# Kernel optimization log

Hardware: AMD Instinct MI355X
Metric: run time of the kernel (lower is better)

Reference implementation:

```python
import jax, jax.numpy as jnp
import numpy as np

EMB_DIM = 1024
NUM_HEADS = 16
HEAD_DIM = EMB_DIM // NUM_HEADS
B, S_Q, S_KV = 4, 2048, 2048


def setup_inputs() -> dict:
    key = jax.random.key(0)
    ks = jax.random.split(key, 12)
    s = EMB_DIM ** -0.5  # torch Linear default init scale (approx, uniform-like)
    inp = {
        "q": jax.random.normal(ks[0], (B, S_Q, EMB_DIM), jnp.float32),
        "k": jax.random.normal(ks[1], (B, S_KV, EMB_DIM), jnp.float32),
        "v": jax.random.normal(ks[2], (B, S_KV, EMB_DIM), jnp.float32),
        "mask": jax.random.randint(ks[3], (B, S_KV), 0, 2, jnp.int32),
        "Wq": jax.random.normal(ks[4], (EMB_DIM, EMB_DIM), jnp.float32) * s,
        "bq": jnp.zeros((EMB_DIM,), jnp.float32),
        "Wk": jax.random.normal(ks[5], (EMB_DIM, EMB_DIM), jnp.float32) * s,
        "bk": jnp.zeros((EMB_DIM,), jnp.float32),
        "Wv": jax.random.normal(ks[6], (EMB_DIM, EMB_DIM), jnp.float32) * s,
        "bv": jnp.zeros((EMB_DIM,), jnp.float32),
        "Wo": jax.random.normal(ks[7], (EMB_DIM, EMB_DIM), jnp.float32) * s,
        "bo": jnp.zeros((EMB_DIM,), jnp.float32),
    }
    return inp


def reference(q, k, v, mask, Wq, bq, Wk, bk, Wv, bv, Wo, bo):
    Bsz, Sq, E = q.shape
    Skv = k.shape[1]
    H, D = NUM_HEADS, HEAD_DIM
    scale = D ** -0.5

    # projections (torch Linear: x @ W.T + b)
    qh = (q @ Wq.T + bq).reshape(Bsz, Sq, H, D).transpose(0, 2, 1, 3)   # [B,H,Sq,D]
    kh = (k @ Wk.T + bk).reshape(Bsz, Skv, H, D).transpose(0, 2, 1, 3)  # [B,H,Skv,D]
    vh = (v @ Wv.T + bv).reshape(Bsz, Skv, H, D).transpose(0, 2, 1, 3)  # [B,H,Skv,D]

    attn = jnp.einsum("bhqd,bhkd->bhqk", qh, kh) * scale  # [B,H,Sq,Skv]

    valid = mask != 0                                      # [B,Skv]
    all_invalid = ~jnp.any(valid, axis=-1, keepdims=True)  # [B,1]
    safe = valid | all_invalid                             # reopened rows
    attn = jnp.where(safe[:, None, None, :], attn, -jnp.inf)

    attn = jax.nn.softmax(attn, axis=-1)
    attn = jnp.where(all_invalid.reshape(Bsz, 1, 1, 1), 0.0, attn)

    out = jnp.einsum("bhqk,bhkd->bhqd", attn, vh)          # [B,H,Sq,D]
    out = out.transpose(0, 2, 1, 3).reshape(Bsz, Sq, E)
    return out @ Wo.T + bo
```

## Files before the change

kernel.cpp:

```cpp
#include <hip/hip_runtime.h>
#include <hip/hip_bf16.h>

typedef short bh8 __attribute__((ext_vector_type(8)));
typedef float f32x4 __attribute__((ext_vector_type(4)));
typedef float f32x16 __attribute__((ext_vector_type(16)));
typedef float f2 __attribute__((ext_vector_type(2)));
typedef unsigned int uint4v __attribute__((ext_vector_type(4)));

#define GLOBAL_P(p) ((const __attribute__((address_space(1))) void*)(p))
#define LDS_P(p)    ((__attribute__((address_space(3))) void*)(p))

__device__ inline bh8 pack8(const float4& a, const float4& b) {
    union { bh8 v; __hip_bfloat16 h[8]; } u;
    u.h[0] = __float2bfloat16(a.x); u.h[1] = __float2bfloat16(a.y);
    u.h[2] = __float2bfloat16(a.z); u.h[3] = __float2bfloat16(a.w);
    u.h[4] = __float2bfloat16(b.x); u.h[5] = __float2bfloat16(b.y);
    u.h[6] = __float2bfloat16(b.z); u.h[7] = __float2bfloat16(b.w);
    return u.v;
}

__global__ __launch_bounds__(256) void cvt1(
    const float* __restrict__ a, __hip_bfloat16* __restrict__ oa)
{
    size_t i = ((size_t)blockIdx.x * 256 + threadIdx.x) * 8;
    float4 x0 = *(const float4*)(a + i), x1 = *(const float4*)(a + i + 4);
    *(bh8*)(oa + i) = pack8(x0, x1);
}

__global__ __launch_bounds__(256) void cvtW(
    const float* __restrict__ a, const float* __restrict__ b,
    const float* __restrict__ c, const float* __restrict__ d,
    __hip_bfloat16* __restrict__ o)
{
    int seg = blockIdx.x >> 9;
    const float* src = (seg == 0) ? a : (seg == 1) ? b : (seg == 2) ? c : d;
    size_t i = ((size_t)(blockIdx.x & 511) * 256 + threadIdx.x) * 8;
    float4 x0 = *(const float4*)(src + i), x1 = *(const float4*)(src + i + 4);
    *(bh8*)(o + (size_t)seg * 1048576 + i) = pack8(x0, x1);
}

__global__ __launch_bounds__(256) void maskScan(
    const int* __restrict__ mask, int* __restrict__ idx, int* __restrict__ nv)
{
    __shared__ int ts[256];
    const int b = blockIdx.x, tid = threadIdx.x;
    int f[8], cnt = 0;
#pragma unroll
    for (int j = 0; j < 8; ++j) {
        f[j] = (mask[b * 2048 + tid * 8 + j] != 0) ? 1 : 0;
        cnt += f[j];
    }
    ts[tid] = cnt;
    __syncthreads();
    for (int off = 1; off < 256; off <<= 1) {
        int v = (tid >= off) ? ts[tid - off] : 0;
        __syncthreads();
        ts[tid] += v;
        __syncthreads();
    }
    int base = ts[tid] - cnt;
#pragma unroll
    for (int j = 0; j < 8; ++j)
        if (f[j]) idx[b * 2048 + base++] = tid * 8 + j;
    if (tid == 255) nv[b] = ts[255];
}

__global__ __launch_bounds__(256) void gatherTok(
    const float* __restrict__ kf, const float* __restrict__ vf,
    const int* __restrict__ idx, const int* __restrict__ nv,
    __hip_bfloat16* __restrict__ kc, __hip_bfloat16* __restrict__ vc)
{
    const int b = blockIdx.x >> 5, rb = blockIdx.x & 31;
    const int n = nv[b], np = (n + 127) & ~127;
    const int r = rb * 64 + (threadIdx.x >> 2);
    if (r >= np) return;
    const int c0 = (threadIdx.x & 3) * 256;
    bh8* dk = (bh8*)(kc + ((size_t)b * 2048 + r) * 1024 + c0);
    bh8* dv = (bh8*)(vc + ((size_t)b * 2048 + r) * 1024 + c0);
    if (r < n) {
        const int s = idx[b * 2048 + r];
        const float4* sk = (const float4*)(kf + ((size_t)b * 2048 + s) * 1024 + c0);
        const float4* sv = (const float4*)(vf + ((size_t)b * 2048 + s) * 1024 + c0);
#pragma unroll
        for (int i = 0; i < 32; ++i) {
            dk[i] = pack8(sk[2 * i], sk[2 * i + 1]);
            dv[i] = pack8(sv[2 * i], sv[2 * i + 1]);
        }
    } else {
        bh8 z = {};
#pragma unroll
        for (int i = 0; i < 32; ++i) { dk[i] = z; dv[i] = z; }
    }
}

template <typename TC, bool COMPACT>
__global__ __launch_bounds__(256) void gemm_bt(
    const __hip_bfloat16* __restrict__ A, const __hip_bfloat16* __restrict__ W,
    const float* __restrict__ bias, TC* __restrict__ C,
    int M, int N, int Ksz, float oscale, const int* __restrict__ nvp)
{
    __shared__ __hip_bfloat16 As[128 * 64];
    __shared__ __hip_bfloat16 Bs[128 * 64];
    const int tid = threadIdx.x;
    const int l = tid & 63, w = tid >> 6;
    const int g4 = l >> 4, rl = l & 15;
    const int nb = N >> 7;
    const int bm = blockIdx.x / nb, bn = blockIdx.x % nb;
    if constexpr (COMPACT) {
        const int np = (nvp[bm >> 4] + 127) & ~127;
        if ((bm & 15) * 128 >= np) return;
    }
    const long m0 = (long)bm * 128, n0 = (long)bn * 128;

    const __hip_bfloat16* ag[4];
    const __hip_bfloat16* wg[4];
    int ldsbase[4];
#pragma unroll
    for (int i = 0; i < 4; ++i) {
        int c = i * 256 + tid;
        int row = c >> 3, c8 = c & 7;
        ag[i] = A + (m0 + row) * Ksz + c8 * 8;
        wg[i] = W + (n0 + row) * Ksz + c8 * 8;
        ldsbase[i] = (i * 256 + w * 64) * 8;
    }

    const int wr = w >> 1, wc = w & 1;
    f32x4 acc[4][4];
#pragma unroll
    for (int i = 0; i < 4; ++i)
#pragma unroll
        for (int j = 0; j < 4; ++j) acc[i][j] = f32x4{0.f, 0.f, 0.f, 0.f};

    const int nk = Ksz >> 6;
    for (int t = 0; t < nk; ++t) {
        __syncthreads();
#pragma unroll
        for (int i = 0; i < 4; ++i) {
            __builtin_amdgcn_global_load_lds(GLOBAL_P(ag[i]), LDS_P((__hip_bfloat16*)As + ldsbase[i]), 16, 0, 0);
            __builtin_amdgcn_global_load_lds(GLOBAL_P(wg[i]), LDS_P((__hip_bfloat16*)Bs + ldsbase[i]), 16, 0, 0);
            ag[i] += 64; wg[i] += 64;
        }
        __syncthreads();
#pragma unroll
        for (int kc = 0; kc < 2; ++kc) {
            bh8 af[4], bf[4];
#pragma unroll
            for (int mt = 0; mt < 4; ++mt) {
                int row = wr * 64 + mt * 16 + rl;
                af[mt] = *(const bh8*)(As + row * 64 + 8 * g4 + 32 * kc);
            }
#pragma unroll
            for (int nt = 0; nt < 4; ++nt) {
                int row = wc * 64 + nt * 16 + rl;
                bf[nt] = *(const bh8*)(Bs + row * 64 + 8 * g4 + 32 * kc);
            }
#pragma unroll
            for (int mt = 0; mt < 4; ++mt)
#pragma unroll
                for (int nt = 0; nt < 4; ++nt)
                    acc[mt][nt] = __builtin_amdgcn_mfma_f32_16x16x32_bf16(af[mt], bf[nt], acc[mt][nt], 0, 0, 0);
        }
    }

    float bv[4];
#pragma unroll
    for (int nt = 0; nt < 4; ++nt)
        bv[nt] = bias[n0 + wc * 64 + nt * 16 + rl];
#pragma unroll
    for (int mt = 0; mt < 4; ++mt) {
#pragma unroll
        for (int r = 0; r < 4; ++r) {
            long row = m0 + wr * 64 + mt * 16 + g4 * 4 + r;
            TC* cp = C + row * N + n0 + wc * 64 + rl;
#pragma unroll
            for (int nt = 0; nt < 4; ++nt) {
                float x = (acc[mt][nt][r] + bv[nt]) * oscale;
                if constexpr (__is_same(TC, float)) cp[nt * 16] = x;
                else cp[nt * 16] = __float2bfloat16(x);
            }
        }
    }
}

#define THRL 11.0f

__global__ __launch_bounds__(256, 2) void attn_kernel(
    const __hip_bfloat16* __restrict__ Qm, const __hip_bfloat16* __restrict__ Km,
    const __hip_bfloat16* __restrict__ Vm, const int* __restrict__ nvp,
    __hip_bfloat16* __restrict__ Om)
{
    __shared__ __hip_bfloat16 Kt[2][64 * 64];
    __shared__ __hip_bfloat16 Vt[2][64 * 64];
    __shared__ float biasS[2048];
    const int tid = threadIdx.x;
    const int w = tid >> 6, l = tid & 63;
    const int G = l >> 5, c = l & 31;
    const int id = blockIdx.x;
    const int xcd = id & 7, slot = id >> 3;
    const int bh = xcd * 8 + (slot >> 4);
    const int qb = slot & 15;
    const int b = bh >> 4, h = bh & 15;
    const int q0 = qb * 128 + w * 32;

    const int n = nvp[b];
    const int nt = (n + 63) >> 6;

#pragma unroll
    for (int i = 0; i < 8; ++i) {
        int idx = i * 256 + tid;
        biasS[idx] = (idx < n) ? 0.f : -1e30f;
    }

    const __hip_bfloat16* qp = Qm + (size_t)(b * 2048 + q0 + c) * 1024 + h * 64 + 8 * G;
    bh8 qf[4];
#pragma unroll
    for (int kc = 0; kc < 4; ++kc) qf[kc] = *(const bh8*)(qp + 16 * kc);

    const int l38 = l >> 3, lc8 = l & 7;
    const __hip_bfloat16* kg0 = Km + (size_t)(b * 2048 + 16 * w + l38) * 1024 + h * 64 + 8 * ((lc8 ^ l38 ^ (2 * w)) & 7);
    const __hip_bfloat16* kg1 = Km + (size_t)(b * 2048 + 16 * w + 8 + l38) * 1024 + h * 64 + 8 * ((lc8 ^ l38 ^ (2 * w + 1)) & 7);
    const int kbase_e = w * 1024;

    const int vpi = tid >> 3, vd0 = (tid & 7) * 8;
    const __hip_bfloat16* vbase = Vm + (size_t)(b * 2048 + 2 * vpi) * 1024 + h * 64 + vd0;

    bh8 va0, va1;
    auto loadV = [&](int tt) {
        const __hip_bfloat16* vp = vbase + (size_t)tt * 64 * 1024;
        va0 = *(const bh8*)vp;
        va1 = *(const bh8*)(vp + 1024);
    };
    auto stageV = [&](int buf) {
        __hip_bfloat16* dst = &Vt[buf][0];
#pragma unroll
        for (int j = 0; j < 8; ++j) {
            int d = vd0 + j;
            int swz = ((d & 7) ^ (d >> 3)) << 3;
            unsigned lo = (unsigned short)((const short*)&va0)[j];
            unsigned hi = (unsigned short)((const short*)&va1)[j];
            *(unsigned*)&dst[(d * 64 + 2 * vpi) ^ swz] = lo | (hi << 16);
        }
    };
    auto stageK = [&](int buf, int tt) {
        const size_t off = (size_t)tt * 64 * 1024;
        __builtin_amdgcn_global_load_lds(GLOBAL_P(kg0 + off), LDS_P(&Kt[buf][0] + kbase_e), 16, 0, 0);
        __builtin_amdgcn_global_load_lds(GLOBAL_P(kg1 + off), LDS_P(&Kt[buf][0] + kbase_e + 512), 16, 0, 0);
    };

    stageK(0, 0);
    loadV(0);
    stageV(0);
    loadV(nt > 1 ? 1 : 0);
    __syncthreads();

    f32x16 o0 = {0.f}, o1 = {0.f};
    float m_run = -1e29f, l_run = 0.f;

    for (int t = 0; t < nt; ++t) {
        const int buf = t & 1;
        if (t < nt - 1) {
            stageK(buf ^ 1, t + 1);
            stageV(buf ^ 1);
            loadV(t + 2 < nt ? t + 2 : nt - 1);
        }
        __builtin_amdgcn_sched_barrier(0);

        const __hip_bfloat16* kbuf = &Kt[buf][0];
        const int kx0 = ((c & 7) ^ (c >> 3)) << 3;
        const int kx1 = kx0 ^ 32;
        f32x16 s0 = {0.f}, s1 = {0.f};
        __builtin_amdgcn_s_setprio(1);
#pragma unroll
        for (int kc = 0; kc < 4; ++kc) {
            bh8 kf = *(const bh8*)(kbuf + c * 64 + ((16 * kc + 8 * G) ^ kx0));
            s0 = __builtin_amdgcn_mfma_f32_32x32x16_bf16(kf, qf[kc], s0, 0, 0, 0);
        }
#pragma unroll
        for (int kc = 0; kc < 4; ++kc) {
            bh8 kf = *(const bh8*)(kbuf + (c + 32) * 64 + ((16 * kc + 8 * G) ^ kx1));
            s1 = __builtin_amdgcn_mfma_f32_32x32x16_bf16(kf, qf[kc], s1, 0, 0, 0);
        }
        __builtin_amdgcn_s_setprio(0);

        f2 mx2 = {-1e30f, -1e30f};
#pragma unroll
        for (int ct = 0; ct < 2; ++ct) {
            f2* sp = (f2*)(ct ? &s1 : &s0);
#pragma unroll
            for (int i2 = 0; i2 < 8; ++i2) {
                const int i = i2 * 2;
                f2 bb = *(const f2*)&biasS[t * 64 + ct * 32 + (i >> 2) * 8 + 4 * G + (i & 3)];
                f2 sv = sp[i2] + bb;
                sp[i2] = sv;
                mx2 = __builtin_elementwise_max(mx2, sv);
            }
        }
        float mxl = fmaxf(mx2[0], mx2[1]);

        if (__all(mxl - m_run <= THRL)) {
            f2 ls2 = {0.f, 0.f};
            f2 m2 = {m_run, m_run};
#pragma unroll
            for (int ct = 0; ct < 2; ++ct) {
                f2* sp = (f2*)(ct ? &s1 : &s0);
#pragma unroll
                for (int i2 = 0; i2 < 8; ++i2) {
                    f2 e = sp[i2] - m2;
                    f2 p;
                    p[0] = __builtin_amdgcn_exp2f(e[0]);
                    p[1] = __builtin_amdgcn_exp2f(e[1]);
                    sp[i2] = p; ls2 += p;
                }
            }
            l_run += ls2[0] + ls2[1];
        } else {
            float mxf = fmaxf(mxl, __shfl_xor(mxl, 32));
            const float m_new = fmaxf(m_run, mxf);
            const float fac = __builtin_amdgcn_exp2f(m_run - m_new);
            f2 ls2 = {0.f, 0.f};
            f2 m2 = {m_new, m_new};
#pragma unroll
            for (int ct = 0; ct < 2; ++ct) {
                f2* sp = (f2*)(ct ? &s1 : &s0);
#pragma unroll
                for (int i2 = 0; i2 < 8; ++i2) {
                    f2 e = sp[i2] - m2;
                    f2 p;
                    p[0] = __builtin_amdgcn_exp2f(e[0]);
                    p[1] = __builtin_amdgcn_exp2f(e[1]);
                    sp[i2] = p; ls2 += p;
                }
            }
            l_run = l_run * fac + (ls2[0] + ls2[1]);
            m_run = m_new;
            f2 fc = {fac, fac};
            f2* o0p = (f2*)&o0; f2* o1p = (f2*)&o1;
#pragma unroll
            for (int i2 = 0; i2 < 8; ++i2) { o0p[i2] *= fc; o1p[i2] *= fc; }
        }

        const __hip_bfloat16* vbuf = &Vt[buf][0];
        const int swz0 = ((c & 7) ^ (c >> 3)) << 3;
        const int swz1 = ((c & 7) ^ ((c + 32) >> 3)) << 3;
#pragma unroll
        for (int sl = 0; sl < 4; ++sl) {
            const f32x16& ps = (sl < 2) ? s0 : s1;
            const int R0 = 8 * (sl & 1);
            unsigned a0, a1, b0, b1;
            asm("v_cvt_pk_bf16_f32 %0, %1, %2" : "=v"(a0) : "v"(ps[R0 + 0]), "v"(ps[R0 + 1]));
            asm("v_cvt_pk_bf16_f32 %0, %1, %2" : "=v"(a1) : "v"(ps[R0 + 2]), "v"(ps[R0 + 3]));
            asm("v_cvt_pk_bf16_f32 %0, %1, %2" : "=v"(b0) : "v"(ps[R0 + 4]), "v"(ps[R0 + 5]));
            asm("v_cvt_pk_bf16_f32 %0, %1, %2" : "=v"(b1) : "v"(ps[R0 + 6]), "v"(ps[R0 + 7]));
            asm("v_permlane32_swap_b32 %0, %1" : "+v"(a0), "+v"(b0));
            asm("v_permlane32_swap_b32 %0, %1" : "+v"(a1), "+v"(b1));
            uint4v pu = {a0, a1, b0, b1};
            bh8 pf = __builtin_bit_cast(bh8, pu);
            const int kvb = 16 * sl + 8 * G;
            bh8 vf0 = *(const bh8*)(vbuf + c * 64 + (kvb ^ swz0));
            bh8 vf1 = *(const bh8*)(vbuf + (c + 32) * 64 + (kvb ^ swz1));
            __builtin_amdgcn_s_setprio(1);
            o0 = __builtin_amdgcn_mfma_f32_32x32x16_bf16(vf0, pf, o0, 0, 0, 0);
            o1 = __builtin_amdgcn_mfma_f32_32x32x16_bf16(vf1, pf, o1, 0, 0, 0);
            __builtin_amdgcn_s_setprio(0);
        }

        __syncthreads();
    }

    float l_tot = l_run + __shfl_xor(l_run, 32);
    float inv = (l_tot > 0.f) ? 1.f / l_tot : 0.f;
    __hip_bfloat16* op = Om + (size_t)(b * 2048 + q0 + c) * 1024 + h * 64 + 4 * G;
#pragma unroll
    for (int dt = 0; dt < 2; ++dt) {
#pragma unroll
        for (int rb = 0; rb < 4; ++rb) {
            union { ushort4 u; __hip_bfloat16 hv[4]; } cv;
#pragma unroll
            for (int j = 0; j < 4; ++j) {
                float x = (dt ? o1[rb * 4 + j] : o0[rb * 4 + j]) * inv;
                cv.hv[j] = __float2bfloat16(x);
            }
            *(ushort4*)(op + dt * 32 + rb * 8) = cv.u;
        }
    }
}

extern "C" void kernel_launch(void* const* d_in, const int* in_sizes, int n_in,
                              void* d_out, int out_size, void* d_ws, size_t ws_size,
                              hipStream_t stream) {
    const float* q  = (const float*)d_in[0];
    const float* k  = (const float*)d_in[1];
    const float* v  = (const float*)d_in[2];
    const int*   mk = (const int*)d_in[3];
    const float* Wq = (const float*)d_in[4];
    const float* bq = (const float*)d_in[5];
    const float* Wk = (const float*)d_in[6];
    const float* bk = (const float*)d_in[7];
    const float* Wv = (const float*)d_in[8];
    const float* bv = (const float*)d_in[9];
    const float* Wo = (const float*)d_in[10];
    const float* bo = (const float*)d_in[11];
    float* out = (float*)d_out;

    const float CSC = 0.18033688011112042f;
    const size_t MN = (size_t)8192 * 1024;
    const size_t WN = (size_t)1024 * 1024;
    __hip_bfloat16* R0 = (__hip_bfloat16*)d_ws;
    __hip_bfloat16* R1 = R0 + MN;
    __hip_bfloat16* R2 = R1 + MN;
    __hip_bfloat16* R3 = R2 + MN;
    __hip_bfloat16* Wb = R3 + MN;
    int* idxp = (int*)(Wb + 4 * WN);
    int* nvp  = idxp + 4 * 2048;

    cvt1<<<4096, 256, 0, stream>>>(q, R0);
    cvtW<<<2048, 256, 0, stream>>>(Wq, Wk, Wv, Wo, Wb);
    maskScan<<<4, 256, 0, stream>>>(mk, idxp, nvp);
    gatherTok<<<128, 256, 0, stream>>>(k, v, idxp, nvp, R1, R2);
    gemm_bt<__hip_bfloat16, false><<<512, 256, 0, stream>>>(R0, Wb,          bq, R3, 8192, 1024, 1024, CSC,  nullptr);
    gemm_bt<__hip_bfloat16, true ><<<512, 256, 0, stream>>>(R1, Wb + WN,     bk, R0, 8192, 1024, 1024, 1.0f, nvp);
    gemm_bt<__hip_bfloat16, true ><<<512, 256, 0, stream>>>(R2, Wb + 2 * WN, bv, R1, 8192, 1024, 1024, 1.0f, nvp);
    attn_kernel<<<1024, 256, 0, stream>>>(R3, R0, R1, nvp, R2);
    gemm_bt<float, false><<<512, 256, 0, stream>>>(R2, Wb + 3 * WN, bo, out, 8192, 1024, 1024, 1.0f, nullptr);
}
```

Baseline: 230.5 us.

## Merge prep kernels, batch Q/K projections in one launch, widen gather grid

Merges the q conversion, weight conversion and mask scan into a single prep launch. Runs the Q and K projection GEMMs as one 1024-block launch so the two can share the GPU, which needs a new workspace buffer (R4) for the K output. Reshapes gatherTok to use 512 blocks with 16 rows each instead of 128 blocks. The aim is to cut launch gaps and tail underutilization. The cost is more workspace and a mixed workload inside one grid.

```diff
diff --git a/kernel.cpp b/kernel.cpp
--- a/kernel.cpp
+++ b/kernel.cpp
@@ -19,50 +19,48 @@
     return u.v;
 }
 
-__global__ __launch_bounds__(256) void cvt1(
-    const float* __restrict__ a, __hip_bfloat16* __restrict__ oa)
-{
-    size_t i = ((size_t)blockIdx.x * 256 + threadIdx.x) * 8;
-    float4 x0 = *(const float4*)(a + i), x1 = *(const float4*)(a + i + 4);
-    *(bh8*)(oa + i) = pack8(x0, x1);
-}
-
-__global__ __launch_bounds__(256) void cvtW(
-    const float* __restrict__ a, const float* __restrict__ b,
-    const float* __restrict__ c, const float* __restrict__ d,
-    __hip_bfloat16* __restrict__ o)
-{
-    int seg = blockIdx.x >> 9;
-    const float* src = (seg == 0) ? a : (seg == 1) ? b : (seg == 2) ? c : d;
-    size_t i = ((size_t)(blockIdx.x & 511) * 256 + threadIdx.x) * 8;
-    float4 x0 = *(const float4*)(src + i), x1 = *(const float4*)(src + i + 4);
-    *(bh8*)(o + (size_t)seg * 1048576 + i) = pack8(x0, x1);
-}
-
-__global__ __launch_bounds__(256) void maskScan(
-    const int* __restrict__ mask, int* __restrict__ idx, int* __restrict__ nv)
+__global__ __launch_bounds__(256) void prep(
+    const float* __restrict__ q, const float* __restrict__ Wq,
+    const float* __restrict__ Wk, const float* __restrict__ Wv,
+    const float* __restrict__ Wo, const int* __restrict__ mask,
+    __hip_bfloat16* __restrict__ qbf, __hip_bfloat16* __restrict__ Wb,
+    int* __restrict__ idx, int* __restrict__ nv)
 {
     __shared__ int ts[256];
-    const int b = blockIdx.x, tid = threadIdx.x;
-    int f[8], cnt = 0;
-#pragma unroll
-    for (int j = 0; j < 8; ++j) {
-        f[j] = (mask[b * 2048 + tid * 8 + j] != 0) ? 1 : 0;
-        cnt += f[j];
-    }
-    ts[tid] = cnt;
-    __syncthreads();
-    for (int off = 1; off < 256; off <<= 1) {
-        int v = (tid >= off) ? ts[tid - off] : 0;
+    const int bid = blockIdx.x, tid = threadIdx.x;
+    if (bid < 4096) {
+        size_t i = ((size_t)bid * 256 + tid) * 8;
+        float4 x0 = *(const float4*)(q + i), x1 = *(const float4*)(q + i + 4);
+        *(bh8*)(qbf + i) = pack8(x0, x1);
+    } else if (bid < 6144) {
+        const int sb = bid - 4096;
+        const int seg = sb >> 9;
+        const float* src = (seg == 0) ? Wq : (seg == 1) ? Wk : (seg == 2) ? Wv : Wo;
+        size_t i = ((size_t)(sb & 511) * 256 + tid) * 8;
+        float4 x0 = *(const float4*)(src + i), x1 = *(const float4*)(src + i + 4);
+        *(bh8*)(Wb + (size_t)seg * 1048576 + i) = pack8(x0, x1);
+    } else {
+        const int b = bid - 6144;
+        int f[8], cnt = 0;
+#pragma unroll
+        for (int j = 0; j < 8; ++j) {
+            f[j] = (mask[b * 2048 + tid * 8 + j] != 0) ? 1 : 0;
+            cnt += f[j];
+        }
+        ts[tid] = cnt;
         __syncthreads();
-        ts[tid] += v;
-        __syncthreads();
-    }
-    int base = ts[tid] - cnt;
-#pragma unroll
-    for (int j = 0; j < 8; ++j)
-        if (f[j]) idx[b * 2048 + base++] = tid * 8 + j;
-    if (tid == 255) nv[b] = ts[255];
+        for (int off = 1; off < 256; off <<= 1) {
+            int v = (tid >= off) ? ts[tid - off] : 0;
+            __syncthreads();
+            ts[tid] += v;
+            __syncthreads();
+        }
+        int base = ts[tid] - cnt;
+#pragma unroll
+        for (int j = 0; j < 8; ++j)
+            if (f[j]) idx[b * 2048 + base++] = tid * 8 + j;
+        if (tid == 255) nv[b] = ts[255];
+    }
 }
 
 __global__ __launch_bounds__(256) void gatherTok(
@@ -70,11 +68,11 @@
     const int* __restrict__ idx, const int* __restrict__ nv,
     __hip_bfloat16* __restrict__ kc, __hip_bfloat16* __restrict__ vc)
 {
-    const int b = blockIdx.x >> 5, rb = blockIdx.x & 31;
+    const int b = blockIdx.x >> 7, rb = blockIdx.x & 127;
     const int n = nv[b], np = (n + 127) & ~127;
-    const int r = rb * 64 + (threadIdx.x >> 2);
+    const int r = rb * 16 + (threadIdx.x >> 4);
     if (r >= np) return;
-    const int c0 = (threadIdx.x & 3) * 256;
+    const int c0 = (threadIdx.x & 15) * 64;
     bh8* dk = (bh8*)(kc + ((size_t)b * 2048 + r) * 1024 + c0);
     bh8* dv = (bh8*)(vc + ((size_t)b * 2048 + r) * 1024 + c0);
     if (r < n) {
@@ -82,34 +80,31 @@
         const float4* sk = (const float4*)(kf + ((size_t)b * 2048 + s) * 1024 + c0);
         const float4* sv = (const float4*)(vf + ((size_t)b * 2048 + s) * 1024 + c0);
 #pragma unroll
-        for (int i = 0; i < 32; ++i) {
+        for (int i = 0; i < 8; ++i) {
             dk[i] = pack8(sk[2 * i], sk[2 * i + 1]);
             dv[i] = pack8(sv[2 * i], sv[2 * i + 1]);
         }
     } else {
         bh8 z = {};
 #pragma unroll
-        for (int i = 0; i < 32; ++i) { dk[i] = z; dv[i] = z; }
+        for (int i = 0; i < 8; ++i) { dk[i] = z; dv[i] = z; }
     }
 }
 
 template <typename TC, bool COMPACT>
-__global__ __launch_bounds__(256) void gemm_bt(
+__device__ __forceinline__ void gemm_core(
     const __hip_bfloat16* __restrict__ A, const __hip_bfloat16* __restrict__ W,
     const float* __restrict__ bias, TC* __restrict__ C,
-    int M, int N, int Ksz, float oscale, const int* __restrict__ nvp)
-{
-    __shared__ __hip_bfloat16 As[128 * 64];
-    __shared__ __hip_bfloat16 Bs[128 * 64];
+    int N, int Ksz, float oscale, const int* __restrict__ nvp,
+    int bm, int bn, __hip_bfloat16* As, __hip_bfloat16* Bs)
+{
+    if constexpr (COMPACT) {
+        const int np = (nvp[bm >> 4] + 127) & ~127;
+        if ((bm & 15) * 128 >= np) return;
+    }
     const int tid = threadIdx.x;
     const int l = tid & 63, w = tid >> 6;
     const int g4 = l >> 4, rl = l & 15;
-    const int nb = N >> 7;
-    const int bm = blockIdx.x / nb, bn = blockIdx.x % nb;
-    if constexpr (COMPACT) {
-        const int np = (nvp[bm >> 4] + 127) & ~127;
-        if ((bm & 15) * 128 >= np) return;
-    }
     const long m0 = (long)bm * 128, n0 = (long)bn * 128;
 
     const __hip_bfloat16* ag[4];
@@ -136,8 +131,8 @@
         __syncthreads();
 #pragma unroll
         for (int i = 0; i < 4; ++i) {
-            __builtin_amdgcn_global_load_lds(GLOBAL_P(ag[i]), LDS_P((__hip_bfloat16*)As + ldsbase[i]), 16, 0, 0);
-            __builtin_amdgcn_global_load_lds(GLOBAL_P(wg[i]), LDS_P((__hip_bfloat16*)Bs + ldsbase[i]), 16, 0, 0);
+            __builtin_amdgcn_global_load_lds(GLOBAL_P(ag[i]), LDS_P(As + ldsbase[i]), 16, 0, 0);
+            __builtin_amdgcn_global_load_lds(GLOBAL_P(wg[i]), LDS_P(Bs + ldsbase[i]), 16, 0, 0);
             ag[i] += 64; wg[i] += 64;
         }
         __syncthreads();
@@ -180,6 +175,36 @@
             }
         }
     }
+}
+
+template <typename TC, bool COMPACT>
+__global__ __launch_bounds__(256) void gemm_bt(
+    const __hip_bfloat16* __restrict__ A, const __hip_bfloat16* __restrict__ W,
+    const float* __restrict__ bias, TC* __restrict__ C,
+    int N, int Ksz, float oscale, const int* __restrict__ nvp)
+{
+    __shared__ __hip_bfloat16 As[128 * 64];
+    __shared__ __hip_bfloat16 Bs[128 * 64];
+    const int nb = N >> 7;
+    gemm_core<TC, COMPACT>(A, W, bias, C, N, Ksz, oscale, nvp,
+                           blockIdx.x / nb, blockIdx.x % nb, As, Bs);
+}
+
+__global__ __launch_bounds__(256) void gemm_projqk(
+    const __hip_bfloat16* __restrict__ Aq, const __hip_bfloat16* __restrict__ Ak,
+    const __hip_bfloat16* __restrict__ Wb, const float* __restrict__ bq,
+    const float* __restrict__ bk, __hip_bfloat16* __restrict__ Cq,
+    __hip_bfloat16* __restrict__ Ck, const int* __restrict__ nvp, float csc)
+{
+    __shared__ __hip_bfloat16 As[128 * 64];
+    __shared__ __hip_bfloat16 Bs[128 * 64];
+    const int bid = blockIdx.x;
+    if (bid < 512)
+        gemm_core<__hip_bfloat16, false>(Aq, Wb, bq, Cq, 1024, 1024, csc, nullptr,
+                                         bid >> 3, bid & 7, As, Bs);
+    else
+        gemm_core<__hip_bfloat16, true>(Ak, Wb + 1048576, bk, Ck, 1024, 1024, 1.0f, nvp,
+                                        (bid - 512) >> 3, bid & 7, As, Bs);
 }
 
 #define THRL 11.0f
@@ -412,14 +437,12 @@
     __hip_bfloat16* Wb = R3 + MN;
     int* idxp = (int*)(Wb + 4 * WN);
     int* nvp  = idxp + 4 * 2048;
-
-    cvt1<<<4096, 256, 0, stream>>>(q, R0);
-    cvtW<<<2048, 256, 0, stream>>>(Wq, Wk, Wv, Wo, Wb);
-    maskScan<<<4, 256, 0, stream>>>(mk, idxp, nvp);
-    gatherTok<<<128, 256, 0, stream>>>(k, v, idxp, nvp, R1, R2);
-    gemm_bt<__hip_bfloat16, false><<<512, 256, 0, stream>>>(R0, Wb,          bq, R3, 8192, 1024, 1024, CSC,  nullptr);
-    gemm_bt<__hip_bfloat16, true ><<<512, 256, 0, stream>>>(R1, Wb + WN,     bk, R0, 8192, 1024, 1024, 1.0f, nvp);
-    gemm_bt<__hip_bfloat16, true ><<<512, 256, 0, stream>>>(R2, Wb + 2 * WN, bv, R1, 8192, 1024, 1024, 1.0f, nvp);
-    attn_kernel<<<1024, 256, 0, stream>>>(R3, R0, R1, nvp, R2);
-    gemm_bt<float, false><<<512, 256, 0, stream>>>(R2, Wb + 3 * WN, bo, out, 8192, 1024, 1024, 1.0f, nullptr);
-}
+    __hip_bfloat16* R4 = (__hip_bfloat16*)((char*)idxp + 33024);
+
+    prep<<<6148, 256, 0, stream>>>(q, Wq, Wk, Wv, Wo, mk, R0, Wb, idxp, nvp);
+    gatherTok<<<512, 256, 0, stream>>>(k, v, idxp, nvp, R1, R2);
+    gemm_projqk<<<1024, 256, 0, stream>>>(R0, R1, Wb, bq, bk, R3, R4, nvp, CSC);
+    gemm_bt<__hip_bfloat16, true><<<512, 256, 0, stream>>>(R2, Wb + 2 * WN, bv, R1, 1024, 1024, 1.0f, nvp);
+    attn_kernel<<<1024, 256, 0, stream>>>(R3, R4, R1, nvp, R0);
+    gemm_bt<float, false><<<512, 256, 0, stream>>>(R0, Wb + 3 * WN, bo, out, 1024, 1024, 1.0f, nullptr);
+}
```

Result: faster. 203.6 us, median of 2 (-11.7%).
